# Kernel tuning notes

Measured on AMD Instinct MI355X. Metric: run time of the kernel, lower is better.

## Reference

```python
import jax, jax.numpy as jnp
import numpy as np

# ---- static config (matches init_kwargs) ----
B, N, D, FH, FW, C = 2, 6, 48, 16, 44, 80
OGH, OGW, DOWNSAMPLE = 256, 704, 16
D_MIN, D_MAX = 2.0, 58.0
XB = (-51.2, 51.2, 0.4); YB = (-51.2, 51.2, 0.4); ZB = (-10.0, 10.0, 20.0)
NX, NY, NZ = 256, 256, 1  # (ub-lb)/step per bound
DX = jnp.array([XB[2], YB[2], ZB[2]], jnp.float32)
LOWER = jnp.array([XB[0], YB[0], ZB[0]], jnp.float32)  # bx - dx/2


def _frustum():
    # UD depth discretization: d_i = d_min + i*(d_max-d_min)/D
    ds = D_MIN + (D_MAX - D_MIN) / D * np.arange(D, dtype=np.float32)
    ds = np.broadcast_to(ds[:, None, None], (D, FH, FW))
    xs = np.broadcast_to(np.linspace(0, OGW - 1, FW, dtype=np.float32)[None, None, :], (D, FH, FW))
    ys = np.broadcast_to(np.linspace(0, OGH - 1, FH, dtype=np.float32)[None, :, None], (D, FH, FW))
    return jnp.asarray(np.stack([xs, ys, ds], -1))  # [D,FH,FW,3]

FRUSTUM = _frustum()


def setup_inputs() -> dict:
    key = jax.random.key(0)
    k1, k2 = jax.random.split(key)
    x = jax.random.normal(k1, (B, N, D, FH, FW, C), dtype=jnp.float32)
    # camera-to-ego rotation: ego_x = z_cam (fwd), ego_y = -x_cam, ego_z = -y_cam
    R = np.array([[0.0, 0.0, 1.0], [-1.0, 0.0, 0.0], [0.0, -1.0, 0.0]], np.float32)
    rots = jnp.asarray(np.broadcast_to(R, (B, N, 3, 3)).copy())
    trans = 2.0 * jax.random.normal(k2, (B, N, 3), dtype=jnp.float32)
    K = np.array([[500.0, 0.0, OGW / 2.0], [0.0, 500.0, OGH / 2.0], [0.0, 0.0, 1.0]], np.float32)
    intrins = jnp.asarray(np.broadcast_to(K, (B, N, 3, 3)).copy())
    post_rots = jnp.asarray(np.broadcast_to(np.eye(3, dtype=np.float32), (B, N, 3, 3)).copy())
    post_trans = jnp.zeros((B, N, 3), jnp.float32)
    return {"x": x, "rots": rots, "trans": trans, "intrins": intrins,
            "post_rots": post_rots, "post_trans": post_trans}


def _get_geometry(rots, trans, intrins, post_rots, post_trans):
    # frustum -> ego-frame 3D points: [B,N,D,FH,FW,3]
    pts = FRUSTUM[None, None] - post_trans[:, :, None, None, None, :]
    inv_post = jnp.linalg.inv(post_rots)
    pts = jnp.einsum('bnij,bndhwj->bndhwi', inv_post, pts)
    # un-normalize pixel coords by depth
    pts = jnp.concatenate([pts[..., :2] * pts[..., 2:3], pts[..., 2:3]], axis=-1)
    combine = jnp.einsum('bnij,bnjk->bnik', rots, jnp.linalg.inv(intrins))
    pts = jnp.einsum('bnij,bndhwj->bndhwi', combine, pts)
    return pts + trans[:, :, None, None, None, :]


def _voxel_pooling(geom, x):
    Nprime = B * N * D * FH * FW
    xf = x.reshape(Nprime, C)
    # voxel indices; torch .long() truncates toward zero -> astype matches
    gi = ((geom.reshape(Nprime, 3) - LOWER) / DX).astype(jnp.int32)
    batch_ix = jnp.repeat(jnp.arange(B, dtype=jnp.int32), Nprime // B)
    kept = ((gi[:, 0] >= 0) & (gi[:, 0] < NX) &
            (gi[:, 1] >= 0) & (gi[:, 1] < NY) &
            (gi[:, 2] >= 0) & (gi[:, 2] < NZ))
    gi = jnp.where(kept[:, None], gi, 0)
    # flat index into (B, NZ, NY, NX); equivalent aggregation to sort+quickcumsum
    flat = ((batch_ix * NZ + gi[:, 2]) * NY + gi[:, 1]) * NX + gi[:, 0]
    xm = jnp.where(kept[:, None], xf, 0.0)
    pooled = jax.ops.segment_sum(xm, flat, num_segments=B * NZ * NY * NX)
    final = pooled.reshape(B, NZ, NY, NX, C).transpose(0, 4, 1, 2, 3)
    return final  # [B, C, NZ, NY, NX]


def reference(x, rots, trans, intrins, post_rots, post_trans):
    geom = _get_geometry(rots, trans, intrins, post_rots, post_trans)
    return _voxel_pooling(geom, x)
```

## Files before the change

### kernel.cpp

```cpp
#include <hip/hip_runtime.h>


#define NCH       80
#define GRID_HW   65536
#define OUT_PER_B 5242880
#define HSTRIDE   3520
#define PTS_PER_BN 33792

#define N_ENT_MAX 405504
#define P_BYTES   129761280u
#define NEXT_OFF  129761280u
#define HEAD_OFF  131383296u
#define CNT_OFF   131907584u
#define WS_NEED   131907588u

__device__ inline void inv3(const double a[9], double inv[9]) {
    double c00 =  a[4]*a[8] - a[5]*a[7];
    double c01 = -(a[3]*a[8] - a[5]*a[6]);
    double c02 =  a[3]*a[7] - a[4]*a[6];
    double det = a[0]*c00 + a[1]*c01 + a[2]*c02;
    double id  = 1.0/det;
    inv[0] = c00*id;
    inv[1] = (a[2]*a[7]-a[1]*a[8])*id;
    inv[2] = (a[1]*a[5]-a[2]*a[4])*id;
    inv[3] = c01*id;
    inv[4] = (a[0]*a[8]-a[2]*a[6])*id;
    inv[5] = (a[2]*a[3]-a[0]*a[5])*id;
    inv[6] = c02*id;
    inv[7] = (a[1]*a[6]-a[0]*a[7])*id;
    inv[8] = (a[0]*a[4]-a[1]*a[3])*id;
}

__device__ inline void prep_bn(const float* __restrict__ rots,
                               const float* __restrict__ trans,
                               const float* __restrict__ intrins,
                               const float* __restrict__ post_rots,
                               const float* __restrict__ post_trans,
                               int bn, double* o) {
    double pr[9], kk[9], rt[9], ipr[9], ik[9];
    #pragma unroll
    for (int i = 0; i < 9; i++) {
        pr[i] = (double)post_rots[bn*9 + i];
        kk[i] = (double)intrins[bn*9 + i];
        rt[i] = (double)rots[bn*9 + i];
    }
    inv3(pr, ipr);
    inv3(kk, ik);
    #pragma unroll
    for (int i = 0; i < 9; i++) o[i] = ipr[i];
    #pragma unroll
    for (int r = 0; r < 3; r++)
        #pragma unroll
        for (int c = 0; c < 3; c++)
            o[9 + r*3 + c] = rt[r*3+0]*ik[0*3+c] + rt[r*3+1]*ik[1*3+c] + rt[r*3+2]*ik[2*3+c];
    #pragma unroll
    for (int i = 0; i < 3; i++) o[18 + i] = (double)post_trans[bn*3 + i];
    #pragma unroll
    for (int i = 0; i < 3; i++) o[21 + i] = (double)trans[bn*3 + i];
}

__global__ void prep_kernel(const float* __restrict__ rots,
                            const float* __restrict__ trans,
                            const float* __restrict__ intrins,
                            const float* __restrict__ post_rots,
                            const float* __restrict__ post_trans,
                            double* __restrict__ tw) {
    int bn = threadIdx.x;
    if (bn >= 12) return;
    prep_bn(rots, trans, intrins, post_rots, post_trans, bn, tw + bn*24);
}

__global__ __launch_bounds__(256) void zero_kernel(float4* __restrict__ p, int n4) {
    int i = blockIdx.x * 256 + threadIdx.x;
    int stride = gridDim.x * 256;
    for (; i < n4; i += stride) p[i] = make_float4(0.f, 0.f, 0.f, 0.f);
}

__global__ __launch_bounds__(256) void init_heads(int* __restrict__ head, int* __restrict__ counter) {
    int i = blockIdx.x * 256 + threadIdx.x;
    if (i < 131072) head[i] = -1;
    if (i == 0) counter[0] = 0;
}

__device__ inline void geom_points(const double* __restrict__ t,
                                   int b, int d, int tid, int* s_base) {
    const float dsv = __fadd_rn(2.0f, __fmul_rn((float)(56.0 / 48.0), (float)d));
    for (int idx = tid; idx < 704; idx += 256) {
        const int h = idx / 44;
        const int w = idx - h * 44;
        float xsv = (w == 43) ? 703.0f : (float)((double)w * (703.0 / 43.0));
        float ysv = (float)(h * 17);

        double px = (double)xsv - t[18];
        double py = (double)ysv - t[19];
        double pz = (double)dsv - t[20];
        double q0 = t[0]*px + t[1]*py + t[2]*pz;
        double q1 = t[3]*px + t[4]*py + t[5]*pz;
        double q2 = t[6]*px + t[7]*py + t[8]*pz;
        q0 *= q2;
        q1 *= q2;
        double e0 = t[9]*q0  + t[10]*q1 + t[11]*q2 + t[21];
        double e1 = t[12]*q0 + t[13]*q1 + t[14]*q2 + t[22];
        double e2 = t[15]*q0 + t[16]*q1 + t[17]*q2 + t[23];

        const double lxy = (double)(-51.2f);
        const double dxy = (double)(0.4f);
        int gx = (int)((e0 - lxy) / dxy);
        int gy = (int)((e1 - lxy) / dxy);
        int gz = (int)((e2 - (double)(-10.0f)) / (double)(20.0f));
        int base = -1;
        if (gx >= 0 && gx < 256 && gy >= 0 && gy < 256 && gz == 0)
            base = (b << 16) | (gy << 8) | gx;
        s_base[idx] = base;
    }
}

__global__ __launch_bounds__(256) void scatter_compact(const float* __restrict__ x,
                                                       const float* __restrict__ rots,
                                                       const float* __restrict__ trans,
                                                       const float* __restrict__ intrins,
                                                       const float* __restrict__ post_rots,
                                                       const float* __restrict__ post_trans,
                                                       float* __restrict__ P,
                                                       int* __restrict__ nxt,
                                                       int* __restrict__ head,
                                                       int* __restrict__ counter) {
    __shared__ double   s_t[24];
    __shared__ int      s_base[704];
    __shared__ int      s_gbase[704];
    __shared__ unsigned s_gmask[704];
    __shared__ int      s_gcount[44];
    __shared__ int      s_goff[44];
    __shared__ short    s_gslot[704];
    __shared__ int      s_eb, s_G;

    const int tid = threadIdx.x;
    const int bn  = blockIdx.x / 48;
    const int d   = blockIdx.x - bn * 48;
    const int b   = bn / 6;

    if (tid == 0)
        prep_bn(rots, trans, intrins, post_rots, post_trans, bn, s_t);
    __syncthreads();

    geom_points(s_t, b, d, tid, s_base);
    __syncthreads();

    if (tid < 44) {
        int gb[16]; unsigned gm[16];
        int cnt = 0;
        #pragma unroll
        for (int h = 0; h < 16; h++) {
            int pb = s_base[h * 44 + tid];
            if (pb >= 0) {
                int j = 0;
                for (; j < cnt; j++) if (gb[j] == pb) break;
                if (j < cnt) gm[j] |= (1u << h);
                else { gb[cnt] = pb; gm[cnt] = (1u << h); cnt++; }
            }
        }
        s_gcount[tid] = cnt;
        for (int j = 0; j < cnt; j++) {
            s_gbase[tid * 16 + j] = gb[j];
            s_gmask[tid * 16 + j] = gm[j];
        }
    }
    __syncthreads();

    if (tid == 0) {
        int off = 0;
        for (int w = 0; w < 44; w++) { s_goff[w] = off; off += s_gcount[w]; }
        s_G  = off;
        s_eb = atomicAdd(counter, off);
    }
    __syncthreads();

    if (tid < 44) {
        int off = s_goff[tid];
        int cnt = s_gcount[tid];
        for (int k = 0; k < cnt; k++) {
            int g = off + k;
            s_gslot[g] = (short)((tid << 4) | k);
            int e = s_eb + g;
            nxt[e] = atomicExch(&head[s_gbase[tid * 16 + k]], e);
        }
    }
    __syncthreads();

    const int G  = s_G;
    const int eb = s_eb;
    const float* xb0 = x + ((size_t)bn * PTS_PER_BN + (size_t)d * 704) * NCH;
    for (int item = tid; item < G * 20; item += 256) {
        int g  = item / 20;
        int c4 = item - g * 20;
        int slot = (int)s_gslot[g];
        int w = slot >> 4;
        int k = slot & 15;
        unsigned mm = s_gmask[w * 16 + k];
        const float* xb = xb0 + (size_t)w * NCH + c4 * 4;
        float ax = 0.f, ay = 0.f, az = 0.f, aw = 0.f;
        #pragma unroll
        for (int h = 0; h < 16; h++) {
            if ((mm >> h) & 1u) {
                float4 v = *(const float4*)(xb + h * HSTRIDE);
                ax += v.x; ay += v.y; az += v.z; aw += v.w;
            }
        }
        float4 r; r.x = ax; r.y = ay; r.z = az; r.w = aw;
        *(float4*)(P + (size_t)(eb + g) * NCH + c4 * 4) = r;
    }
}

__global__ __launch_bounds__(256) void gather_kernel(const float* __restrict__ P,
                                                     const int* __restrict__ nxt,
                                                     const int* __restrict__ head,
                                                     float* __restrict__ out) {
    __shared__ float tile[64 * 81];
    const int tid = threadIdx.x;
    const int b   = blockIdx.x >> 10;
    const int v0  = (blockIdx.x & 1023) * 64;
    const int* hb = head + (b << 16) + v0;
    #pragma unroll
    for (int i = 0; i < 20; i++) {
        int j = i * 256 + tid;
        int v = j / 80;
        int c = j - v * 80;
        float s = 0.f;
        int e = hb[v];
        while (e >= 0) {
            s += P[(size_t)e * NCH + c];
            e = nxt[e];
        }
        tile[v * 81 + c] = s;
    }
    __syncthreads();
    float* dst = out + (size_t)b * OUT_PER_B + v0;
    #pragma unroll
    for (int i = 0; i < 20; i++) {
        int k  = i * 256 + tid;
        int c  = k >> 6;
        int lv = k & 63;
        dst[(size_t)c * GRID_HW + lv] = tile[lv * 81 + c];
    }
}

__global__ __launch_bounds__(256) void scatter_direct_kernel(const float* __restrict__ x,
                                                             const double* __restrict__ ws,
                                                             float* __restrict__ out) {
    __shared__ int      s_base[704];
    __shared__ int      s_colbase[44];
    __shared__ unsigned s_mask[44];
    __shared__ unsigned s_fb[44];

    const int tid = threadIdx.x;
    const int bn  = blockIdx.x / 48;
    const int d   = blockIdx.x - bn * 48;
    const int b   = bn / 6;
    geom_points(ws + bn * 24, b, d, tid, s_base);
    __syncthreads();

    if (tid < 44) {
        int cb = -1; unsigned mm = 0, fb = 0;
        #pragma unroll
        for (int h = 0; h < 16; h++) {
            int pb = s_base[h * 44 + tid];
            if (pb >= 0) {
                if (cb < 0) cb = pb;
                if (pb == cb) mm |= (1u << h);
                else          fb |= (1u << h);
            }
        }
        s_colbase[tid] = cb;
        s_mask[tid]    = mm;
        s_fb[tid]      = fb;
    }
    __syncthreads();

    const float* xb0 = x + ((size_t)bn * PTS_PER_BN + (size_t)d * 704) * NCH;
    #pragma unroll
    for (int pass = 0; pass < 4; pass++) {
        int item = pass * 256 + tid;
        if (item >= 880) break;
        int w  = item / 20;
        int c4 = item - w * 20;
        unsigned mm = s_mask[w];
        unsigned fb = s_fb[w];
        if (!(mm | fb)) continue;
        const float* xb = xb0 + (size_t)w * NCH + c4 * 4;
        float ax = 0.f, ay = 0.f, az = 0.f, aw = 0.f;
        #pragma unroll
        for (int h = 0; h < 16; h++) {
            if ((mm >> h) & 1u) {
                float4 v = *(const float4*)(xb + h * HSTRIDE);
                ax += v.x; ay += v.y; az += v.z; aw += v.w;
            } else if ((fb >> h) & 1u) {
                float4 v = *(const float4*)(xb + h * HSTRIDE);
                int vb = s_base[h * 44 + w];
                float* o = out + (size_t)(vb >> 16) * OUT_PER_B + (vb & 65535);
                atomicAdd(o + (size_t)(c4*4 + 0) * GRID_HW, v.x);
                atomicAdd(o + (size_t)(c4*4 + 1) * GRID_HW, v.y);
                atomicAdd(o + (size_t)(c4*4 + 2) * GRID_HW, v.z);
                atomicAdd(o + (size_t)(c4*4 + 3) * GRID_HW, v.w);
            }
        }
        if (mm) {
            int vb = s_colbase[w];
            float* o = out + (size_t)(vb >> 16) * OUT_PER_B + (vb & 65535);
            atomicAdd(o + (size_t)(c4*4 + 0) * GRID_HW, ax);
            atomicAdd(o + (size_t)(c4*4 + 1) * GRID_HW, ay);
            atomicAdd(o + (size_t)(c4*4 + 2) * GRID_HW, az);
            atomicAdd(o + (size_t)(c4*4 + 3) * GRID_HW, aw);
        }
    }
}

extern "C" void kernel_launch(void* const* d_in, const int* in_sizes, int n_in,
                              void* d_out, int out_size, void* d_ws, size_t ws_size,
                              hipStream_t stream) {
    const float* x          = (const float*)d_in[0];
    const float* rots       = (const float*)d_in[1];
    const float* trans      = (const float*)d_in[2];
    const float* intrins    = (const float*)d_in[3];
    const float* post_rots  = (const float*)d_in[4];
    const float* post_trans = (const float*)d_in[5];
    float* out = (float*)d_out;

    if (ws_size >= (size_t)WS_NEED) {
        float* P       = (float*)d_ws;
        int*   nxt     = (int*)((char*)d_ws + NEXT_OFF);
        int*   head    = (int*)((char*)d_ws + HEAD_OFF);
        int*   counter = (int*)((char*)d_ws + CNT_OFF);
        init_heads<<<512, 256, 0, stream>>>(head, counter);
        scatter_compact<<<576, 256, 0, stream>>>(x, rots, trans, intrins,
                                                 post_rots, post_trans,
                                                 P, nxt, head, counter);
        gather_kernel<<<2048, 256, 0, stream>>>(P, nxt, head, out);
    } else if (ws_size >= 12 * 24 * sizeof(double)) {
        double* tw = (double*)d_ws;
        zero_kernel<<<2560, 256, 0, stream>>>((float4*)out, out_size / 16);
        prep_kernel<<<1, 64, 0, stream>>>(rots, trans, intrins, post_rots, post_trans, tw);
        scatter_direct_kernel<<<576, 256, 0, stream>>>(x, tw, out);
    }
}
```

Baseline: 250.5 us.

## Split scatter into geometry grouping and grid-stride reduce kernel over entries

The old compact-scatter kernel did both geometry grouping and the per-entry feature reduction inside the same 576 blocks. It is now two kernels: one computes groups and writes packed per-entry metadata (slice, column, row mask), and a separate 2048-block grid-stride kernel sums features across all entries. This is meant to fix load imbalance and low parallelism in the reduction. The reduce loop now loads all 16 rows unconditionally and masks them with FMAs, and the gather kernel caches heads in shared memory. The costs are an extra launch, a metadata buffer, and reading up to 16x more x data per entry, since masked rows are still loaded.

```diff
diff --git a/kernel.cpp b/kernel.cpp
--- a/kernel.cpp
+++ b/kernel.cpp
@@ -12,7 +12,8 @@
 #define NEXT_OFF  129761280u
 #define HEAD_OFF  131383296u
 #define CNT_OFF   131907584u
-#define WS_NEED   131907588u
+#define META_OFF  131907840u
+#define WS_NEED   133529856u
 
 __device__ inline void inv3(const double a[9], double inv[9]) {
     double c00 =  a[4]*a[8] - a[5]*a[7];
@@ -115,29 +116,28 @@
     }
 }
 
-__global__ __launch_bounds__(256) void scatter_compact(const float* __restrict__ x,
-                                                       const float* __restrict__ rots,
-                                                       const float* __restrict__ trans,
-                                                       const float* __restrict__ intrins,
-                                                       const float* __restrict__ post_rots,
-                                                       const float* __restrict__ post_trans,
-                                                       float* __restrict__ P,
-                                                       int* __restrict__ nxt,
-                                                       int* __restrict__ head,
-                                                       int* __restrict__ counter) {
+__global__ __launch_bounds__(256) void geom_groups(const float* __restrict__ rots,
+                                                   const float* __restrict__ trans,
+                                                   const float* __restrict__ intrins,
+                                                   const float* __restrict__ post_rots,
+                                                   const float* __restrict__ post_trans,
+                                                   int* __restrict__ nxt,
+                                                   int* __restrict__ head,
+                                                   int* __restrict__ counter,
+                                                   unsigned* __restrict__ ent_meta) {
     __shared__ double   s_t[24];
     __shared__ int      s_base[704];
     __shared__ int      s_gbase[704];
     __shared__ unsigned s_gmask[704];
     __shared__ int      s_gcount[44];
     __shared__ int      s_goff[44];
-    __shared__ short    s_gslot[704];
-    __shared__ int      s_eb, s_G;
-
-    const int tid = threadIdx.x;
-    const int bn  = blockIdx.x / 48;
-    const int d   = blockIdx.x - bn * 48;
-    const int b   = bn / 6;
+    __shared__ int      s_eb;
+
+    const int tid   = threadIdx.x;
+    const int slice = blockIdx.x;
+    const int bn    = slice / 48;
+    const int d     = slice - bn * 48;
+    const int b     = bn / 6;
 
     if (tid == 0)
         prep_bn(rots, trans, intrins, post_rots, post_trans, bn, s_t);
@@ -170,7 +170,6 @@
     if (tid == 0) {
         int off = 0;
         for (int w = 0; w < 44; w++) { s_goff[w] = off; off += s_gcount[w]; }
-        s_G  = off;
         s_eb = atomicAdd(counter, off);
     }
     __syncthreads();
@@ -179,35 +178,42 @@
         int off = s_goff[tid];
         int cnt = s_gcount[tid];
         for (int k = 0; k < cnt; k++) {
-            int g = off + k;
-            s_gslot[g] = (short)((tid << 4) | k);
-            int e = s_eb + g;
+            int e = s_eb + off + k;
+            ent_meta[e] = ((unsigned)slice << 22) | ((unsigned)tid << 16)
+                        | (s_gmask[tid * 16 + k] & 0xFFFFu);
             nxt[e] = atomicExch(&head[s_gbase[tid * 16 + k]], e);
         }
     }
-    __syncthreads();
-
-    const int G  = s_G;
-    const int eb = s_eb;
-    const float* xb0 = x + ((size_t)bn * PTS_PER_BN + (size_t)d * 704) * NCH;
-    for (int item = tid; item < G * 20; item += 256) {
-        int g  = item / 20;
-        int c4 = item - g * 20;
-        int slot = (int)s_gslot[g];
-        int w = slot >> 4;
-        int k = slot & 15;
-        unsigned mm = s_gmask[w * 16 + k];
-        const float* xb = xb0 + (size_t)w * NCH + c4 * 4;
+}
+
+__global__ __launch_bounds__(256) void reduce_kernel(const float* __restrict__ x,
+                                                     const unsigned* __restrict__ ent_meta,
+                                                     const int* __restrict__ counter,
+                                                     float* __restrict__ P) {
+    const int NE = counter[0];
+    const int total = NE * 20;
+    int i = blockIdx.x * 256 + threadIdx.x;
+    const int stride = gridDim.x * 256;
+    for (; i < total; i += stride) {
+        int e  = i / 20;
+        int c4 = i - e * 20;
+        unsigned meta = ent_meta[e];
+        int slice   = (int)(meta >> 22);
+        int w       = (int)((meta >> 16) & 63u);
+        unsigned mm = meta & 0xFFFFu;
+        const float* xb = x + (size_t)(slice * 704 + w) * NCH + c4 * 4;
         float ax = 0.f, ay = 0.f, az = 0.f, aw = 0.f;
         #pragma unroll
         for (int h = 0; h < 16; h++) {
-            if ((mm >> h) & 1u) {
-                float4 v = *(const float4*)(xb + h * HSTRIDE);
-                ax += v.x; ay += v.y; az += v.z; aw += v.w;
-            }
+            float4 v = *(const float4*)(xb + h * HSTRIDE);
+            float m = (float)((mm >> h) & 1u);
+            ax = fmaf(m, v.x, ax);
+            ay = fmaf(m, v.y, ay);
+            az = fmaf(m, v.z, az);
+            aw = fmaf(m, v.w, aw);
         }
         float4 r; r.x = ax; r.y = ay; r.z = az; r.w = aw;
-        *(float4*)(P + (size_t)(eb + g) * NCH + c4 * 4) = r;
+        *(float4*)(P + (size_t)e * NCH + c4 * 4) = r;
     }
 }
 
@@ -216,17 +222,18 @@
                                                      const int* __restrict__ head,
                                                      float* __restrict__ out) {
     __shared__ float tile[64 * 81];
+    __shared__ int   s_head[64];
     const int tid = threadIdx.x;
     const int b   = blockIdx.x >> 10;
     const int v0  = (blockIdx.x & 1023) * 64;
-    const int* hb = head + (b << 16) + v0;
-    #pragma unroll
+    if (tid < 64) s_head[tid] = head[(b << 16) + v0 + tid];
+    __syncthreads();
     for (int i = 0; i < 20; i++) {
         int j = i * 256 + tid;
         int v = j / 80;
         int c = j - v * 80;
         float s = 0.f;
-        int e = hb[v];
+        int e = s_head[v];
         while (e >= 0) {
             s += P[(size_t)e * NCH + c];
             e = nxt[e];
@@ -326,14 +333,16 @@
     float* out = (float*)d_out;
 
     if (ws_size >= (size_t)WS_NEED) {
-        float* P       = (float*)d_ws;
-        int*   nxt     = (int*)((char*)d_ws + NEXT_OFF);
-        int*   head    = (int*)((char*)d_ws + HEAD_OFF);
-        int*   counter = (int*)((char*)d_ws + CNT_OFF);
+        float*    P       = (float*)d_ws;
+        int*      nxt     = (int*)((char*)d_ws + NEXT_OFF);
+        int*      head    = (int*)((char*)d_ws + HEAD_OFF);
+        int*      counter = (int*)((char*)d_ws + CNT_OFF);
+        unsigned* meta    = (unsigned*)((char*)d_ws + META_OFF);
         init_heads<<<512, 256, 0, stream>>>(head, counter);
-        scatter_compact<<<576, 256, 0, stream>>>(x, rots, trans, intrins,
-                                                 post_rots, post_trans,
-                                                 P, nxt, head, counter);
+        geom_groups<<<576, 256, 0, stream>>>(rots, trans, intrins,
+                                             post_rots, post_trans,
+                                             nxt, head, counter, meta);
+        reduce_kernel<<<2048, 256, 0, stream>>>(x, meta, counter, P);
         gather_kernel<<<2048, 256, 0, stream>>>(P, nxt, head, out);
     } else if (ws_size >= 12 * 24 * sizeof(double)) {
         double* tw = (double*)d_ws;
```

New measurement: 240.4 us. -4.0%, faster.
